# Kernel optimization log

Measured on AMD Instinct MI355X. Metric: run time of the kernel, lower is better.

The kernel has to match this reference:

```python
import jax, jax.numpy as jnp
import numpy as np


def _kernel_mean(x, y, beta):
    # mean of exp(-beta * ||x_i - y_j||^2) over all pairs, without cdist call:
    x2 = jnp.sum(x * x, axis=1)  # [B1]
    y2 = jnp.sum(y * y, axis=1)  # [B2]
    d2 = x2[:, None] + y2[None, :] - 2.0 * jnp.einsum('id,jd->ij', x, y)
    d2 = jnp.maximum(d2, 0.0)
    return jnp.mean(jnp.exp(-beta * d2))


def setup_inputs() -> dict:
    key = jax.random.key(0)
    k1, k2 = jax.random.split(key)
    source = jax.random.normal(k1, (8192, 256), dtype=jnp.float32)
    target = jax.random.normal(k2, (8192, 256), dtype=jnp.float32)
    return {"source": source, "target": target}


def reference(source, target):
    sigma = 1.0
    beta = 1.0 / (2.0 * sigma)
    if source.ndim > 2:
        source = source.reshape(source.shape[0], -1)
    if target.ndim > 2:
        target = target.reshape(target.shape[0], -1)
    k_ss = _kernel_mean(source, source, beta)
    k_tt = _kernel_mean(target, target, beta)
    k_st = _kernel_mean(source, target, beta)
    return k_ss + k_tt - 2.0 * k_st
```

## Files before the change

### kernel.cpp

```cpp
#include <hip/hip_runtime.h>
#include <hip/hip_bf16.h>

#define NROWS 8192
#define DIM 256
#define NT 32
#define TRI ((NT * (NT + 1)) / 2)
#define NBLK (2 * TRI + NT * NT)

typedef __attribute__((ext_vector_type(8))) short short8;
typedef __attribute__((ext_vector_type(4))) float f32x4;

__device__ __forceinline__ ushort f2bf(float f) {
  unsigned u = __float_as_uint(f);
  u += 0x7fffu + ((u >> 16) & 1u);
  return (ushort)(u >> 16);
}
__device__ __forceinline__ float bf2f(ushort b) {
  return __uint_as_float(((unsigned)b) << 16);
}

#define NEGHALF_LOG2E (-0.72134752044448170368f)
#define LOG2E          (1.44269504088896340736f)

__global__ __launch_bounds__(256) void prep_kernel(
    const float* __restrict__ S, const float* __restrict__ T,
    ushort* __restrict__ Sb, ushort* __restrict__ Tb,
    float* __restrict__ x2s, float* __restrict__ x2t,
    float* __restrict__ accums) {
  if (blockIdx.x == 0 && threadIdx.x == 0) accums[0] = 0.f;
  const int w = threadIdx.x >> 6, l = threadIdx.x & 63;
  const int r = blockIdx.x * 4 + w;
  const float* src;
  ushort* dst;
  float* sq;
  int row;
  if (r < NROWS) { src = S; dst = Sb; sq = x2s; row = r; }
  else           { src = T; dst = Tb; sq = x2t; row = r - NROWS; }

  const float4 v = *(const float4*)(src + (size_t)row * DIM + l * 4);
  float vf[4] = {v.x, v.y, v.z, v.w};
  ushort b[4];
  float s = 0.f;
#pragma unroll
  for (int i = 0; i < 4; ++i) {
    b[i] = f2bf(vf[i]);
    float f = bf2f(b[i]);
    s += f * f;
  }
  *(ushort4*)(dst + (size_t)row * DIM + l * 4) = make_ushort4(b[0], b[1], b[2], b[3]);
#pragma unroll
  for (int off = 32; off > 0; off >>= 1) s += __shfl_xor(s, off);
  if (l == 0) sq[row] = s * NEGHALF_LOG2E;
}

__device__ __forceinline__ void gload_lds16(const void* g, void* lds) {
  __builtin_amdgcn_global_load_lds(
      (const __attribute__((address_space(1))) unsigned int*)g,
      (__attribute__((address_space(3))) unsigned int*)lds, 16, 0, 0);
}

__global__ __launch_bounds__(512, 2) void mmd_gemm(
    const ushort* __restrict__ Sb, const ushort* __restrict__ Tb,
    const float* __restrict__ x2s, const float* __restrict__ x2t,
    float* __restrict__ accums) {
  __shared__ __align__(16) ushort lA[2][256 * 32];
  __shared__ __align__(16) ushort lB[2][256 * 32];
  __shared__ float lAx2[256];
  __shared__ float lBx2[256];
  __shared__ float wsum[8];

  const int tid = threadIdx.x;
  const int l = tid & 63;
  const int w = tid >> 6;
  const int wr = w >> 2, wc = w & 3;

  const int bid = blockIdx.x;
  const ushort* Ap;
  const ushort* Bp;
  const float* a2;
  const float* b2;
  int tr, tc;
  float wgt;
  if (bid < 2 * TRI) {
    const int i = (bid < TRI) ? bid : bid - TRI;
    int g = (int)((sqrtf((float)(8 * i + 1)) - 1.0f) * 0.5f);
    g = min(max(g - 2, 0), NT - 1);
    tr = g;
    while (tr < NT - 1 && (tr + 1) * (tr + 2) / 2 <= i) ++tr;
    tc = i - tr * (tr + 1) / 2;
    wgt = (tr == tc) ? 1.f : 2.f;
    if (bid < TRI) { Ap = Sb; Bp = Sb; a2 = x2s; b2 = x2s; }
    else           { Ap = Tb; Bp = Tb; a2 = x2t; b2 = x2t; }
  } else {
    const int t = bid - 2 * TRI;
    tr = t >> 5; tc = t & 31;
    wgt = -2.f;
    Ap = Sb; Bp = Tb; a2 = x2s; b2 = x2t;
  }

  const ushort* gA = Ap + (size_t)(tr * 256) * DIM;
  const ushort* gB = Bp + (size_t)(tc * 256) * DIM;

  if (tid < 256) lAx2[tid] = a2[tr * 256 + tid];
  else           lBx2[tid - 256] = b2[tc * 256 + tid - 256];

  f32x4 acc[8][4];
  const f32x4 zero = {0.f, 0.f, 0.f, 0.f};
#pragma unroll
  for (int m = 0; m < 8; ++m)
#pragma unroll
    for (int n = 0; n < 4; ++n) acc[m][n] = zero;

#define STAGE(buf, k0)                                                     \
  {                                                                        \
    _Pragma("unroll")                                                      \
    for (int j = 0; j < 2; ++j) {                                          \
      const int c = j * 512 + tid;                                         \
      const int row_ = c >> 2, kc_ = c & 3;                                \
      gload_lds16(gA + (size_t)row_ * DIM + (k0) + kc_ * 8, &lA[buf][c * 8]); \
      gload_lds16(gB + (size_t)row_ * DIM + (k0) + kc_ * 8, &lB[buf][c * 8]); \
    }                                                                      \
  }

#define COMPUTE(buf)                                                       \
  {                                                                        \
    short8 af[8], bfv[4];                                                  \
    _Pragma("unroll")                                                      \
    for (int m = 0; m < 8; ++m) {                                          \
      const int row_ = wr * 128 + m * 16 + (l & 15);                       \
      af[m] = *(const short8*)&lA[buf][row_ * 32 + (l >> 4) * 8];          \
    }                                                                      \
    _Pragma("unroll")                                                      \
    for (int n = 0; n < 4; ++n) {                                          \
      const int row_ = wc * 64 + n * 16 + (l & 15);                        \
      bfv[n] = *(const short8*)&lB[buf][row_ * 32 + (l >> 4) * 8];         \
    }                                                                      \
    __builtin_amdgcn_s_setprio(1);                                         \
    _Pragma("unroll")                                                      \
    for (int m = 0; m < 8; ++m)                                            \
      _Pragma("unroll")                                                    \
      for (int n = 0; n < 4; ++n)                                          \
        acc[m][n] = __builtin_amdgcn_mfma_f32_16x16x32_bf16(               \
            af[m], bfv[n], acc[m][n], 0, 0, 0);                            \
    __builtin_amdgcn_s_setprio(0);                                         \
  }

  STAGE(0, 0);
#pragma unroll
  for (int ks = 0; ks < 8; ++ks) {
    const int cur = ks & 1;
    if (ks < 7) {
      STAGE(cur ^ 1, (ks + 1) * 32);
      asm volatile("s_waitcnt vmcnt(4)" ::: "memory");
    } else {
      asm volatile("s_waitcnt vmcnt(0)" ::: "memory");
    }
    __builtin_amdgcn_s_barrier();
    asm volatile("" ::: "memory");
    COMPUTE(cur);
    asm volatile("" ::: "memory");
    __builtin_amdgcn_s_barrier();
  }

  float cb[4];
#pragma unroll
  for (int n = 0; n < 4; ++n) cb[n] = lBx2[wc * 64 + n * 16 + (l & 15)];
  float local = 0.f;
#pragma unroll
  for (int m = 0; m < 8; ++m) {
#pragma unroll
    for (int j = 0; j < 4; ++j) {
      const float rc = lAx2[wr * 128 + m * 16 + ((l >> 4) * 4 + j)];
#pragma unroll
      for (int n = 0; n < 4; ++n) {
        float arg = fmaf(LOG2E, acc[m][n][j], rc + cb[n]);
        arg = fminf(arg, 0.f);
        local += exp2f(arg);
      }
    }
  }
#pragma unroll
  for (int off = 32; off > 0; off >>= 1) local += __shfl_xor(local, off);
  if (l == 0) wsum[w] = local;
  __syncthreads();
  if (tid == 0) {
    float tot = 0.f;
#pragma unroll
    for (int i = 0; i < 8; ++i) tot += wsum[i];
    atomicAdd(&accums[0], tot * wgt);
  }
}

__global__ void finalize_kernel(const float* __restrict__ accums, float* __restrict__ out) {
  out[0] = accums[0] * (1.f / ((float)NROWS * (float)NROWS));
}

extern "C" void kernel_launch(void* const* d_in, const int* in_sizes, int n_in,
                              void* d_out, int out_size, void* d_ws, size_t ws_size,
                              hipStream_t stream) {
  const float* S = (const float*)d_in[0];
  const float* T = (const float*)d_in[1];
  float* out = (float*)d_out;

  ushort* Sb = (ushort*)d_ws;
  ushort* Tb = Sb + (size_t)NROWS * DIM;
  float* x2s = (float*)(Tb + (size_t)NROWS * DIM);
  float* x2t = x2s + NROWS;
  float* accums = x2t + NROWS;

  prep_kernel<<<(2 * NROWS) / 4, 256, 0, stream>>>(S, T, Sb, Tb, x2s, x2t, accums);
  mmd_gemm<<<NBLK, 512, 0, stream>>>(Sb, Tb, x2s, x2t, accums);
  finalize_kernel<<<1, 1, 0, stream>>>(accums, out);
}
```

Baseline: 184.2 us.

## Triple-buffer GEMM K-loop with XOR-swizzled LDS and split-stage prefetch

Replaces the double-buffered K loop with a three-buffer pipeline that prefetches two k-tiles ahead. It also splits each iteration into two halves, issuing half of the next-next tile's loads in each half. The LDS layout of the A/B tiles gets an XOR swizzle on the 16-byte column chunk to cut bank conflicts on the ds_read_b128 fragment loads. The extra buffer raises LDS use per block to about 96KB, which may stop two blocks from sharing a CU as the launch bounds intend.

```diff
diff --git a/kernel.cpp b/kernel.cpp
--- a/kernel.cpp
+++ b/kernel.cpp
@@ -63,8 +63,8 @@
     const ushort* __restrict__ Sb, const ushort* __restrict__ Tb,
     const float* __restrict__ x2s, const float* __restrict__ x2t,
     float* __restrict__ accums) {
-  __shared__ __align__(16) ushort lA[2][256 * 32];
-  __shared__ __align__(16) ushort lB[2][256 * 32];
+  __shared__ __align__(16) ushort lA[3][256 * 32];
+  __shared__ __align__(16) ushort lB[3][256 * 32];
   __shared__ float lAx2[256];
   __shared__ float lBx2[256];
   __shared__ float wsum[8];
@@ -101,6 +101,20 @@
   const ushort* gA = Ap + (size_t)(tr * 256) * DIM;
   const ushort* gB = Bp + (size_t)(tc * 256) * DIM;
 
+#define STAGE2(kt, jj)                                                     \
+  {                                                                        \
+    const int c_ = (jj) * 512 + tid;                                       \
+    const int row_ = c_ >> 2, sp_ = c_ & 3;                                \
+    const int sl_ = sp_ ^ ((row_ >> 1) & 3);                               \
+    const int buf_ = (kt) % 3;                                             \
+    const size_t go_ = (size_t)row_ * DIM + (kt) * 32 + sl_ * 8;           \
+    gload_lds16(gA + go_, &lA[buf_][c_ * 8]);                              \
+    gload_lds16(gB + go_, &lB[buf_][c_ * 8]);                              \
+  }
+
+  STAGE2(0, 0); STAGE2(0, 1);
+  STAGE2(1, 0); STAGE2(1, 1);
+
   if (tid < 256) lAx2[tid] = a2[tr * 256 + tid];
   else           lBx2[tid - 256] = b2[tc * 256 + tid - 256];
 
@@ -111,55 +125,52 @@
 #pragma unroll
     for (int n = 0; n < 4; ++n) acc[m][n] = zero;
 
-#define STAGE(buf, k0)                                                     \
-  {                                                                        \
-    _Pragma("unroll")                                                      \
-    for (int j = 0; j < 2; ++j) {                                          \
-      const int c = j * 512 + tid;                                         \
-      const int row_ = c >> 2, kc_ = c & 3;                                \
-      gload_lds16(gA + (size_t)row_ * DIM + (k0) + kc_ * 8, &lA[buf][c * 8]); \
-      gload_lds16(gB + (size_t)row_ * DIM + (k0) + kc_ * 8, &lB[buf][c * 8]); \
-    }                                                                      \
-  }
-
-#define COMPUTE(buf)                                                       \
-  {                                                                        \
-    short8 af[8], bfv[4];                                                  \
-    _Pragma("unroll")                                                      \
-    for (int m = 0; m < 8; ++m) {                                          \
-      const int row_ = wr * 128 + m * 16 + (l & 15);                       \
-      af[m] = *(const short8*)&lA[buf][row_ * 32 + (l >> 4) * 8];          \
-    }                                                                      \
-    _Pragma("unroll")                                                      \
-    for (int n = 0; n < 4; ++n) {                                          \
-      const int row_ = wc * 64 + n * 16 + (l & 15);                        \
-      bfv[n] = *(const short8*)&lB[buf][row_ * 32 + (l >> 4) * 8];         \
-    }                                                                      \
-    __builtin_amdgcn_s_setprio(1);                                         \
-    _Pragma("unroll")                                                      \
-    for (int m = 0; m < 8; ++m)                                            \
-      _Pragma("unroll")                                                    \
-      for (int n = 0; n < 4; ++n)                                          \
-        acc[m][n] = __builtin_amdgcn_mfma_f32_16x16x32_bf16(               \
-            af[m], bfv[n], acc[m][n], 0, 0, 0);                            \
-    __builtin_amdgcn_s_setprio(0);                                         \
-  }
-
-  STAGE(0, 0);
-#pragma unroll
-  for (int ks = 0; ks < 8; ++ks) {
-    const int cur = ks & 1;
-    if (ks < 7) {
-      STAGE(cur ^ 1, (ks + 1) * 32);
-      asm volatile("s_waitcnt vmcnt(4)" ::: "memory");
-    } else {
-      asm volatile("s_waitcnt vmcnt(0)" ::: "memory");
-    }
+#pragma unroll
+  for (int kt = 0; kt < 8; ++kt) {
+    const int cur = kt % 3;
+    if (kt == 7) { asm volatile("s_waitcnt vmcnt(0)" ::: "memory"); }
+    else         { asm volatile("s_waitcnt vmcnt(4)" ::: "memory"); }
     __builtin_amdgcn_s_barrier();
     asm volatile("" ::: "memory");
-    COMPUTE(cur);
+
+    if (kt < 6) STAGE2(kt + 2, 0);
+    short8 bfv[4], af[4];
+#pragma unroll
+    for (int n = 0; n < 4; ++n) {
+      const int row = wc * 64 + n * 16 + (l & 15);
+      const int sp = (l >> 4) ^ ((row >> 1) & 3);
+      bfv[n] = *(const short8*)&lB[cur][row * 32 + sp * 8];
+    }
+#pragma unroll
+    for (int m = 0; m < 4; ++m) {
+      const int row = wr * 128 + m * 16 + (l & 15);
+      const int sp = (l >> 4) ^ ((row >> 1) & 3);
+      af[m] = *(const short8*)&lA[cur][row * 32 + sp * 8];
+    }
+    __builtin_amdgcn_s_setprio(1);
+#pragma unroll
+    for (int m = 0; m < 4; ++m)
+#pragma unroll
+      for (int n = 0; n < 4; ++n)
+        acc[m][n] = __builtin_amdgcn_mfma_f32_16x16x32_bf16(af[m], bfv[n], acc[m][n], 0, 0, 0);
+    __builtin_amdgcn_s_setprio(0);
+    __builtin_amdgcn_s_barrier();
     asm volatile("" ::: "memory");
-    __builtin_amdgcn_s_barrier();
+
+    if (kt < 6) STAGE2(kt + 2, 1);
+#pragma unroll
+    for (int m = 0; m < 4; ++m) {
+      const int row = wr * 128 + 64 + m * 16 + (l & 15);
+      const int sp = (l >> 4) ^ ((row >> 1) & 3);
+      af[m] = *(const short8*)&lA[cur][row * 32 + sp * 8];
+    }
+    __builtin_amdgcn_s_setprio(1);
+#pragma unroll
+    for (int m = 0; m < 4; ++m)
+#pragma unroll
+      for (int n = 0; n < 4; ++n)
+        acc[4 + m][n] = __builtin_amdgcn_mfma_f32_16x16x32_bf16(af[m], bfv[n], acc[4 + m][n], 0, 0, 0);
+    __builtin_amdgcn_s_setprio(0);
   }
 
   float cb[4];
```

Result: no change. 181.4 us (-1.5%).
